# Kernel tuning notes

Hardware: AMD Instinct MI355X
Metric: run time of the kernel (lower is better)

Reference implementation:

```python
import jax, jax.numpy as jnp
import numpy as np

NEG_SLOPE = 0.2  # PyG GATv2 default negative_slope


def _gru_last(x, W_ih, W_hh, b_ih, b_hh):
    """x: [B, T, Hin] -> final GRU hidden state [B, H] (torch nn.GRU equations)."""
    gx = x @ W_ih.T + b_ih  # [B, T, 3H], input gates precomputed
    H = W_hh.shape[1]

    def step(h, g):
        gh = h @ W_hh.T + b_hh
        xr, xz, xn = jnp.split(g, 3, axis=-1)
        hr, hz, hn = jnp.split(gh, 3, axis=-1)
        r = jax.nn.sigmoid(xr + hr)
        z = jax.nn.sigmoid(xz + hz)
        n = jnp.tanh(xn + r * hn)
        return (1.0 - z) * n + z * h, None

    h0 = jnp.zeros((x.shape[0], H), x.dtype)
    hT, _ = jax.lax.scan(step, h0, jnp.swapaxes(gx, 0, 1))
    return hT


def _conv(x, w, b, stride):
    y = jax.lax.conv_general_dilated(x, w, (stride, stride), 'SAME',
                                     dimension_numbers=('NCHW', 'OIHW', 'NCHW'))
    return jax.nn.relu(y + b[None, :, None, None])


def _forward(obs, phase, obs_map, edges, edges_feature, params):
    (W_nbrs, b_nbrs, W_ih, W_hh, b_ih, b_hh, Wl, Wr, att_a, gat_bias,
     conv1_w, conv1_b, conv2_w, conv2_b, Wc, bc, Wp, bp, Wh, bh,
     Wo, bo, Wa, ba) = params
    B, N = obs.shape[0], obs.shape[1]
    BN = B * N
    heads, C = att_a.shape

    # per-node obs embedding (MLP) + GRU over seq -> last hidden
    x = jax.nn.relu(obs.reshape(BN, obs.shape[2], obs.shape[3]) @ W_nbrs + b_nbrs)
    h = _gru_last(x, W_ih, W_hh, b_ih, b_hh)  # [BN, hidden]

    # flat_edges: offset each sample's node ids by b*N, concat along edge dim
    offsets = (jnp.arange(B) * N)[:, None, None]
    ei = (edges + offsets).transpose(1, 0, 2).reshape(2, -1)  # [2, B*E]
    loops = jnp.arange(BN)  # PyG GATv2 add_self_loops=True
    src = jnp.concatenate([ei[0], loops])
    dst = jnp.concatenate([ei[1], loops])

    # GATv2Conv (heads, concat=False): gather -> leakyrelu -> edge softmax -> scatter
    xl = (h @ Wl).reshape(BN, heads, C)
    xr = (h @ Wr).reshape(BN, heads, C)
    e = jax.nn.leaky_relu(xl[src] + xr[dst], NEG_SLOPE)  # [Etot, heads, C]
    logits = jnp.einsum('ehc,hc->eh', e, att_a)          # [Etot, heads]
    m = jax.ops.segment_max(logits, dst, num_segments=BN)
    p = jnp.exp(logits - m[dst])
    s = jax.ops.segment_sum(p, dst, num_segments=BN)
    alpha = p / s[dst]                                    # [Etot, heads]
    node_out = jax.ops.segment_sum(xl[src] * alpha[..., None], dst, num_segments=BN)
    obs_gat = node_out.mean(axis=1) + gat_bias            # concat=False -> head mean

    source_idx = jnp.arange(B) * N  # ego intersection of each sample
    obs_gat = obs_gat[source_idx]   # [B, hidden]

    # CNNBase on map
    c = _conv(obs_map, conv1_w, conv1_b, 2)
    c = _conv(c, conv2_w, conv2_b, 2)
    target_emb = jax.nn.relu(c.reshape(B, -1) @ Wc + bc)

    # phase MLP, fusion MLP, dueling head
    phase_emb = jax.nn.relu(phase @ Wp + bp)
    fused = jnp.concatenate([obs_gat, target_emb, phase_emb], axis=1)
    hid = jax.nn.relu(fused @ Wh + bh)
    v = hid @ Wo + bo
    adv = hid @ Wa + ba
    out = v + (adv - adv.mean(axis=-1, keepdims=True))
    return out, alpha


def setup_inputs() -> dict:
    key = jax.random.key(0)
    B, N, T, Fo = 16, 1000, 16, 16      # batch, n_nodes, seq_len, obs_length+4
    H, heads, P, A, E = 128, 5, 8, 8, 4000
    Cm, HW = 4, 32
    ks = iter(jax.random.split(key, 40))

    def rn(shape, scale=0.05):
        return jax.random.normal(next(ks), shape, dtype=jnp.float32) * scale

    return dict(
        obs=rn((B, N, T, Fo), 1.0),
        phase=rn((B, P), 1.0),
        obs_map=rn((B, Cm, HW, HW), 1.0),
        edges=jax.random.randint(next(ks), (B, 2, E), 0, N),
        edges_feature=rn((B, E, 4), 1.0),
        W_nbrs=rn((Fo, H)), b_nbrs=jnp.zeros((H,), jnp.float32),
        W_ih=rn((3 * H, H)), W_hh=rn((3 * H, H)),
        b_ih=jnp.zeros((3 * H,), jnp.float32), b_hh=jnp.zeros((3 * H,), jnp.float32),
        Wl=rn((H, heads * H)), Wr=rn((H, heads * H)),
        att_a=rn((heads, H)), gat_bias=jnp.zeros((H,), jnp.float32),
        conv1_w=rn((32, Cm, 3, 3)), conv1_b=jnp.zeros((32,), jnp.float32),
        conv2_w=rn((64, 32, 3, 3)), conv2_b=jnp.zeros((64,), jnp.float32),
        Wc=rn((64 * (HW // 4) * (HW // 4), H)), bc=jnp.zeros((H,), jnp.float32),
        Wp=rn((P, P)), bp=jnp.zeros((P,), jnp.float32),
        Wh=rn((2 * H + P, H)), bh=jnp.zeros((H,), jnp.float32),
        Wo=rn((H, 1)), bo=jnp.zeros((1,), jnp.float32),
        Wa=rn((H, A)), ba=jnp.zeros((A,), jnp.float32),
    )


def reference(obs, phase, obs_map, edges, edges_feature,
              W_nbrs, b_nbrs, W_ih, W_hh, b_ih, b_hh,
              Wl, Wr, att_a, gat_bias,
              conv1_w, conv1_b, conv2_w, conv2_b, Wc, bc,
              Wp, bp, Wh, bh, Wo, bo, Wa, ba):
    params = (W_nbrs, b_nbrs, W_ih, W_hh, b_ih, b_hh, Wl, Wr, att_a, gat_bias,
              conv1_w, conv1_b, conv2_w, conv2_b, Wc, bc, Wp, bp, Wh, bh,
              Wo, bo, Wa, ba)
    return _forward(obs, phase, obs_map, edges, edges_feature, params)
```

## Files before the change

### kernel.cpp

```cpp
#include <hip/hip_runtime.h>
#include <hip/hip_bf16.h>
#include <math.h>

#define B_    16
#define N_    1000
#define BN_   16000
#define T_    16
#define FO    16
#define H_    128
#define G3    384
#define HEADS 5
#define HC    640
#define E_    4000
#define EG    64000
#define ETOT  80000
#define P_    8
#define A_    8
#define NEG_SLOPE 0.2f

typedef __attribute__((ext_vector_type(8))) short bf16x8;
typedef __attribute__((ext_vector_type(4))) float f32x4;

__device__ __forceinline__ float bf2f(unsigned short u){ return __uint_as_float(((unsigned)u)<<16); }
__device__ __forceinline__ unsigned short f2bf(float x){
    unsigned u = __float_as_uint(x);
    unsigned r = (u + 0x7FFFu + ((u>>16)&1u)) >> 16;
    return (unsigned short)r;
}
__device__ __forceinline__ unsigned cvtpk(float lo, float hi){
    unsigned r;
    asm volatile("v_cvt_pk_bf16_f32 %0, %1, %2" : "=v"(r) : "v"(lo), "v"(hi));
    return r;
}
__device__ __forceinline__ float rcpf(float x){ return __builtin_amdgcn_rcpf(x); }

__global__ __launch_bounds__(256) void k_prep_c1(
        const float* __restrict__ Wih, const float* __restrict__ Whh,
        const float* __restrict__ Wl, const float* __restrict__ Wr,
        const float* __restrict__ Wn, const float* __restrict__ bn,
        unsigned short* __restrict__ Wihb, unsigned short* __restrict__ Whhb,
        unsigned short* __restrict__ WTb, unsigned short* __restrict__ WnTb,
        float* __restrict__ segsum, float* __restrict__ node_out,
        float* __restrict__ tacc,
        const float* __restrict__ im, const float* __restrict__ w1,
        const float* __restrict__ b1, float* __restrict__ c1out){
    __shared__ float sW[32*4*9];
    int t = threadIdx.x;
    if(blockIdx.x < 640){
        int i = blockIdx.x*256 + t;
        if(i < G3*H_){ Wihb[i] = f2bf(Wih[i]); Whhb[i] = f2bf(Whh[i]); }
        if(i < 2*HC*H_){
            int c = i >> 7, k = i & 127;
            float v = (c < HC) ? Wl[(size_t)k*HC + c] : Wr[(size_t)k*HC + (c-HC)];
            WTb[i] = f2bf(v);
        }
        if(i < H_*32){
            int c = i >> 5, k = i & 31;
            WnTb[i] = (k < FO) ? f2bf(Wn[k*H_ + c])
                     : (k == FO ? f2bf(bn[c]) : (unsigned short)0);
        }
        if(i < BN_*HEADS) segsum[i] = 0.0f;
        if(i < B_*HC) node_out[i] = 0.0f;
        if(i < B_*H_) tacc[i] = 0.0f;
    } else {
        for(int i=t;i<32*4*9;i+=256) sW[i]=w1[i];
        __syncthreads();
        int idx = (blockIdx.x-640)*256 + t;
        int ox = idx & 15, oy = (idx>>4)&15, oc = (idx>>8)&31, b = idx>>13;
        float acc = b1[oc];
        for(int ic=0;ic<4;ic++){
            const float* ip = &im[(size_t)((b*4+ic)*32)*32];
            const float* wp = &sW[(oc*4+ic)*9];
            #pragma unroll
            for(int ky=0;ky<3;ky++){
                int iy = oy*2+ky; if(iy>=32) continue;
                #pragma unroll
                for(int kx=0;kx<3;kx++){
                    int ix = ox*2+kx; if(ix>=32) continue;
                    acc = fmaf(ip[iy*32+ix], wp[ky*3+kx], acc);
                }
            }
        }
        c1out[idx] = fmaxf(acc, 0.f);
    }
}

__global__ __launch_bounds__(512,2) void k_gruf(const float* __restrict__ obs,
        const unsigned short* __restrict__ WnTb,
        const unsigned short* __restrict__ Wihb, const float* __restrict__ bih,
        const unsigned short* __restrict__ Whhb, const float* __restrict__ bhh,
        unsigned short* __restrict__ hout,
        const float* __restrict__ c1, const float* __restrict__ w2,
        const float* __restrict__ b2, float* __restrict__ c2out){
    __shared__ unsigned short sX[2*8192];
    __shared__ unsigned short sH[2*8192];
    int t = threadIdx.x;

    if(blockIdx.x >= 250){
        int idx = (blockIdx.x-250)*512 + t;
        int ox = idx & 7, oy = (idx>>3)&7, oc = (idx>>6)&63, b = idx>>12;
        float acc = b2[oc];
        for(int ic=0;ic<32;ic++){
            const float* ip = &c1[(size_t)((b*32+ic)*16)*16];
            const float* wp = &w2[(oc*32+ic)*9];
            #pragma unroll
            for(int ky=0;ky<3;ky++){
                int iy = oy*2+ky; if(iy>=16) continue;
                #pragma unroll
                for(int kx=0;kx<3;kx++){
                    int ix = ox*2+kx; if(ix>=16) continue;
                    acc = fmaf(ip[iy*16+ix], wp[ky*3+kx], acc);
                }
            }
        }
        c2out[idx] = fmaxf(acc, 0.f);
        return;
    }

    int w = t>>6, lane = t&63, lq = lane>>4, lm = lane&15;

    bf16x8 wfi[3][4], wfh[3][4];
    #pragma unroll
    for(int i=0;i<3;i++){
        int row = (8*i + w)*16 + lm;
        #pragma unroll
        for(int kt=0;kt<4;kt++){
            wfi[i][kt] = *(const bf16x8*)&Wihb[row*H_ + kt*32 + lq*8];
            wfh[i][kt] = *(const bf16x8*)&Whhb[row*H_ + kt*32 + lq*8];
        }
    }
    bf16x8 wfn = *(const bf16x8*)&WnTb[(w*16+lm)*32 + lq*8];
    int cb = w*16 + lq*4;
    f32x4 b_r, b_z, bxn, bhn;
    { f32x4 t1=*(const f32x4*)&bih[cb],     t2=*(const f32x4*)&bhh[cb];     b_r=t1+t2; }
    { f32x4 t1=*(const f32x4*)&bih[128+cb], t2=*(const f32x4*)&bhh[128+cb]; b_z=t1+t2; }
    bxn = *(const f32x4*)&bih[256+cb];
    bhn = *(const f32x4*)&bhh[256+cb];

    int rd[4];
    #pragma unroll
    for(int kt=0;kt<4;kt++) rd[kt] = lm*128 + (((4*kt+lq)^(lm&7))<<3);
    const int wrt = lm*128 + (((2*w + (lq>>1))^(lm&7))<<3) + ((lq&1)<<2);

    int nodeBase = blockIdx.x*64;
    const float* obp0 = &obs[(size_t)(nodeBase + lm)*256 + lq*8];

    for(int i=t;i<4096;i+=512) ((unsigned*)sH)[i] = 0u;
    float ho[4][4] = {{0.f,0.f,0.f,0.f},{0.f,0.f,0.f,0.f},
                      {0.f,0.f,0.f,0.f},{0.f,0.f,0.f,0.f}};

    float4 oA[4], oB[4];
    if(lq < 2){
        #pragma unroll
        for(int g=0; g<4; g++){
            const float* q = obp0 + (size_t)g*16*256;
            oA[g] = *(const float4*)(q);    oB[g] = *(const float4*)(q+4);
        }
    }
    #pragma unroll
    for(int g=0; g<4; g++){
        bf16x8 ob = (bf16x8){0,0,0,0,0,0,0,0};
        if(lq < 2){
            union { uint4 u; bf16x8 v; } cv;
            cv.u = make_uint4(cvtpk(oA[g].x,oA[g].y), cvtpk(oA[g].z,oA[g].w),
                              cvtpk(oB[g].x,oB[g].y), cvtpk(oB[g].z,oB[g].w));
            ob = cv.v;
        } else if(lq == 2){
            ob[0] = (short)0x3F80;
        }
        f32x4 xa = (f32x4){0.f,0.f,0.f,0.f};
        xa = __builtin_amdgcn_mfma_f32_16x16x32_bf16(wfn, ob, xa, 0,0,0);
        unsigned u0 = cvtpk(fmaxf(xa[0],0.f), fmaxf(xa[1],0.f));
        unsigned u1 = cvtpk(fmaxf(xa[2],0.f), fmaxf(xa[3],0.f));
        *(uint2*)&sX[g*2048 + wrt] = make_uint2(u0,u1);
    }
    __syncthreads();

    int p = 0;
    #pragma unroll 1
    for(int s=0; s<T_; s++){
        if(s < T_-1 && lq < 2){
            #pragma unroll
            for(int g=0; g<4; g++){
                const float* q = obp0 + (size_t)g*16*256 + (s+1)*16;
                oA[g] = *(const float4*)(q);    oB[g] = *(const float4*)(q+4);
            }
        }
        #pragma unroll
        for(int g=0; g<4; g++){
            int base = p*8192 + g*2048;
            bf16x8 xb[4], hb[4];
            #pragma unroll
            for(int kt=0;kt<4;kt++){
                xb[kt] = *(const bf16x8*)&sX[base + rd[kt]];
                hb[kt] = *(const bf16x8*)&sH[base + rd[kt]];
            }
            f32x4 ar = b_r, az = b_z, axi = bxn, ahh = bhn;
            #pragma unroll
            for(int kt=0;kt<4;kt++){
                ar  = __builtin_amdgcn_mfma_f32_16x16x32_bf16(wfi[0][kt], xb[kt], ar, 0,0,0);
                az  = __builtin_amdgcn_mfma_f32_16x16x32_bf16(wfi[1][kt], xb[kt], az, 0,0,0);
                axi = __builtin_amdgcn_mfma_f32_16x16x32_bf16(wfi[2][kt], xb[kt], axi, 0,0,0);
                ar  = __builtin_amdgcn_mfma_f32_16x16x32_bf16(wfh[0][kt], hb[kt], ar, 0,0,0);
                az  = __builtin_amdgcn_mfma_f32_16x16x32_bf16(wfh[1][kt], hb[kt], az, 0,0,0);
                ahh = __builtin_amdgcn_mfma_f32_16x16x32_bf16(wfh[2][kt], hb[kt], ahh, 0,0,0);
            }
            #pragma unroll
            for(int v=0;v<4;v++){
                float er = __expf(-ar[v]);
                float r  = rcpf(1.f + er);
                float ez = __expf(-az[v]);
                float z  = rcpf(1.f + ez);
                float xn = fmaf(r, ahh[v], axi[v]);
                float en = __expf(-2.f*xn);
                float nn = fmaf(2.f, rcpf(1.f + en), -1.f);
                ho[g][v] = nn + z*(ho[g][v] - nn);
            }
            unsigned u0 = cvtpk(ho[g][0], ho[g][1]);
            unsigned u1 = cvtpk(ho[g][2], ho[g][3]);
            *(uint2*)&sH[(p^1)*8192 + g*2048 + wrt] = make_uint2(u0,u1);
        }
        if(s < T_-1){
            #pragma unroll
            for(int g=0; g<4; g++){
                bf16x8 ob = (bf16x8){0,0,0,0,0,0,0,0};
                if(lq < 2){
                    union { uint4 u; bf16x8 v; } cv;
                    cv.u = make_uint4(cvtpk(oA[g].x,oA[g].y), cvtpk(oA[g].z,oA[g].w),
                                      cvtpk(oB[g].x,oB[g].y), cvtpk(oB[g].z,oB[g].w));
                    ob = cv.v;
                } else if(lq == 2){
                    ob[0] = (short)0x3F80;
                }
                f32x4 xa = (f32x4){0.f,0.f,0.f,0.f};
                xa = __builtin_amdgcn_mfma_f32_16x16x32_bf16(wfn, ob, xa, 0,0,0);
                unsigned u0 = cvtpk(fmaxf(xa[0],0.f), fmaxf(xa[1],0.f));
                unsigned u1 = cvtpk(fmaxf(xa[2],0.f), fmaxf(xa[3],0.f));
                *(uint2*)&sX[(p^1)*8192 + g*2048 + wrt] = make_uint2(u0,u1);
            }
        }
        __syncthreads();
        p ^= 1;
    }
    #pragma unroll
    for(int g=0; g<4; g++){
        unsigned u0 = cvtpk(ho[g][0], ho[g][1]);
        unsigned u1 = cvtpk(ho[g][2], ho[g][3]);
        *(uint2*)&hout[(size_t)(nodeBase + g*16 + lm)*H_ + cb] = make_uint2(u0,u1);
    }
}

__global__ __launch_bounds__(256) void k_xlxr(const unsigned short* __restrict__ hb16,
        const unsigned short* __restrict__ WTb,
        unsigned short* __restrict__ xl, unsigned short* __restrict__ xr){
    int t = threadIdx.x;
    int w = t>>6, lane = t&63, lq = lane>>4, lm = lane&15;
    int nb = blockIdx.x / 5, cgrp = blockIdx.x % 5;
    int nblk = nb*128;
    int ct0 = cgrp*16 + w*4;
    bf16x8 wf[4][4];
    #pragma unroll
    for(int i=0;i<4;i++){
        int row = (ct0+i)*16 + lm;
        #pragma unroll
        for(int kt=0;kt<4;kt++)
            wf[i][kt] = *(const bf16x8*)&WTb[(size_t)row*H_ + kt*32 + lq*8];
    }
    for(int g=0; g<8; g++){
        int node = nblk + g*16 + lm;
        bf16x8 hb[4];
        #pragma unroll
        for(int kt=0;kt<4;kt++)
            hb[kt] = *(const bf16x8*)&hb16[(size_t)node*H_ + kt*32 + lq*8];
        f32x4 acc[4];
        #pragma unroll
        for(int i=0;i<4;i++) acc[i] = (f32x4){0.f,0.f,0.f,0.f};
        #pragma unroll
        for(int kt=0;kt<4;kt++){
            #pragma unroll
            for(int i=0;i<4;i++)
                acc[i] = __builtin_amdgcn_mfma_f32_16x16x32_bf16(wf[i][kt], hb[kt], acc[i], 0,0,0);
        }
        #pragma unroll
        for(int i=0;i<4;i++){
            int col = (ct0+i)*16 + lq*4;
            ushort4 o;
            o.x=f2bf(acc[i][0]); o.y=f2bf(acc[i][1]); o.z=f2bf(acc[i][2]); o.w=f2bf(acc[i][3]);
            if(col < HC) *(ushort4*)&xl[(size_t)node*HC + col] = o;
            else         *(ushort4*)&xr[(size_t)node*HC + (col-HC)] = o;
        }
    }
}

__device__ __forceinline__ void edge_sd(int e, const int* __restrict__ edges, int* src, int* dst){
    if(e < EG){
        int b = e / E_, j = e - b*E_;
        *src = edges[(b*2+0)*E_ + j] + b*N_;
        *dst = edges[(b*2+1)*E_ + j] + b*N_;
    } else { *src = *dst = e - EG; }
}

__global__ __launch_bounds__(256) void k_logits_tb(const unsigned short* __restrict__ xl,
        const unsigned short* __restrict__ xr, const int* __restrict__ edges,
        const float* __restrict__ atta, float* __restrict__ pbuf,
        float* __restrict__ segsum,
        const float* __restrict__ c2, const float* __restrict__ Wc,
        float* __restrict__ tacc){
    __shared__ float sC[128];
    int t = threadIdx.x;
    if(blockIdx.x < 5000){
        int lb = (blockIdx.x & 7)*625 + (blockIdx.x >> 3);
        int lane = t & 63, w = t >> 6;
        float am[8], a4[8];
        #pragma unroll
        for(int j=0;j<8;j++) am[j] = atta[lane*8+j];
        #pragma unroll
        for(int j=0;j<8;j++) a4[j] = (lane<16) ? atta[512+lane*8+j] : 0.f;

        int e0 = lb*16 + w*4;
        int srcs[4], dsts[4];
        #pragma unroll
        for(int i=0;i<4;i++) edge_sd(e0+i, edges, &srcs[i], &dsts[i]);
        #pragma unroll
        for(int i=0;i<4;i++){
            const unsigned short* xls = &xl[(size_t)srcs[i]*HC];
            const unsigned short* xrd = &xr[(size_t)dsts[i]*HC];
            uint4 ul = *(const uint4*)&xls[lane*8];
            uint4 ur = *(const uint4*)&xrd[lane*8];
            uint4 tl = make_uint4(0,0,0,0), tr = make_uint4(0,0,0,0);
            if(lane < 16){
                tl = *(const uint4*)&xls[512+lane*8];
                tr = *(const uint4*)&xrd[512+lane*8];
            }
            float pm = 0.f, p4 = 0.f;
            {
                unsigned pl[4] = {ul.x,ul.y,ul.z,ul.w};
                unsigned pr[4] = {ur.x,ur.y,ur.z,ur.w};
                #pragma unroll
                for(int q=0;q<4;q++){
                    float s0 = bf2f((unsigned short)(pl[q]&0xFFFFu)) + bf2f((unsigned short)(pr[q]&0xFFFFu));
                    float s1 = bf2f((unsigned short)(pl[q]>>16))     + bf2f((unsigned short)(pr[q]>>16));
                    s0 = s0 > 0.f ? s0 : NEG_SLOPE*s0;
                    s1 = s1 > 0.f ? s1 : NEG_SLOPE*s1;
                    pm = fmaf(s0, am[2*q],   pm);
                    pm = fmaf(s1, am[2*q+1], pm);
                }
            }
            {
                unsigned ql[4] = {tl.x,tl.y,tl.z,tl.w};
                unsigned qr[4] = {tr.x,tr.y,tr.z,tr.w};
                #pragma unroll
                for(int q=0;q<4;q++){
                    float s0 = bf2f((unsigned short)(ql[q]&0xFFFFu)) + bf2f((unsigned short)(qr[q]&0xFFFFu));
                    float s1 = bf2f((unsigned short)(ql[q]>>16))     + bf2f((unsigned short)(qr[q]>>16));
                    s0 = s0 > 0.f ? s0 : NEG_SLOPE*s0;
                    s1 = s1 > 0.f ? s1 : NEG_SLOPE*s1;
                    p4 = fmaf(s0, a4[2*q],   p4);
                    p4 = fmaf(s1, a4[2*q+1], p4);
                }
            }
            #pragma unroll
            for(int off=1; off<16; off<<=1){
                pm += __shfl_xor(pm, off);
                p4 += __shfl_xor(p4, off);
            }
            if((lane & 15) == 0){
                int hh = lane >> 4;
                float p = __expf(pm);
                pbuf[(size_t)(e0+i)*HEADS + hh] = p;
                atomicAdd(&segsum[dsts[i]*HEADS + hh], p);
            }
            if(lane == 8){
                float p = __expf(p4);
                pbuf[(size_t)(e0+i)*HEADS + 4] = p;
                atomicAdd(&segsum[dsts[i]*HEADS + 4], p);
            }
        }
    } else {
        int bb = blockIdx.x - 5000;
        int b = bb >> 5, ks = bb & 31;
        int k0 = ks*128;
        if(t < 128) sC[t] = c2[(size_t)b*4096 + k0 + t];
        __syncthreads();
        int j = t & 127, sub = t >> 7;
        const float* wp = &Wc[(size_t)(k0 + sub*64)*H_ + j];
        const float* cp = &sC[sub*64];
        float a0=0.f, a1=0.f, a2=0.f, a3=0.f;
        #pragma unroll
        for(int kk=0; kk<64; kk+=4){
            a0 = fmaf(cp[kk+0], wp[(size_t)(kk+0)*H_], a0);
            a1 = fmaf(cp[kk+1], wp[(size_t)(kk+1)*H_], a1);
            a2 = fmaf(cp[kk+2], wp[(size_t)(kk+2)*H_], a2);
            a3 = fmaf(cp[kk+3], wp[(size_t)(kk+3)*H_], a3);
        }
        atomicAdd(&tacc[b*H_+j], (a0+a1)+(a2+a3));
    }
}

__global__ void k_alpha(const float* __restrict__ pbuf, const float* __restrict__ segsum,
                        const int* __restrict__ edges, const unsigned short* __restrict__ xl,
                        float* __restrict__ out_alpha, float* __restrict__ node_out){
    int idx = blockIdx.x*256 + threadIdx.x;
    int lane = threadIdx.x & 63;
    bool valid = idx < ETOT*HEADS;
    int e = 0, hh = 0, src = 0, dst = 0;
    float a = 0.f;
    bool ego = false;
    if(valid){
        e = idx / HEADS; hh = idx - e*HEADS;
        edge_sd(e, edges, &src, &dst);
        a = pbuf[idx] / segsum[dst*HEADS + hh];
        out_alpha[idx] = a;
        ego = (dst % N_) == 0;
    }
    unsigned long long m = __ballot(ego);
    while(m){
        int l = __ffsll((unsigned long long)m) - 1;
        m &= (m - 1);
        float aa = __shfl(a, l);
        int ss = __shfl(src, l), dd = __shfl(dst, l), hq = __shfl(hh, l);
        int b = dd / N_;
        unsigned u = *(const unsigned*)&xl[(size_t)ss*HC + hq*H_ + lane*2];
        float* no = &node_out[b*HC + hq*H_ + lane*2];
        atomicAdd(no,     aa * bf2f((unsigned short)(u & 0xFFFFu)));
        atomicAdd(no + 1, aa * bf2f((unsigned short)(u >> 16)));
    }
}

__global__ __launch_bounds__(256) void k_head(const float* __restrict__ node_out,
        const float* __restrict__ gat_bias, const float* __restrict__ tacc,
        const float* __restrict__ bc, const float* __restrict__ phase,
        const float* __restrict__ Wp, const float* __restrict__ bp,
        const float* __restrict__ Wh, const float* __restrict__ bh,
        const float* __restrict__ Wo, const float* __restrict__ bo,
        const float* __restrict__ Wa, const float* __restrict__ ba,
        float* __restrict__ out){
    __shared__ float sF[268];
    __shared__ float sHid[128];
    int t = threadIdx.x;
    int b = blockIdx.x;
    if(t < 128){
        float s=0.f;
        #pragma unroll
        for(int hh=0;hh<HEADS;hh++) s += node_out[b*HC + hh*H_ + t];
        sF[t] = s*(1.0f/HEADS) + gat_bias[t];
    } else {
        int c = t - 128;
        sF[128+c] = fmaxf(tacc[b*H_ + c] + bc[c], 0.f);
    }
    if(t < P_){
        float s=bp[t];
        #pragma unroll
        for(int q=0;q<P_;q++) s = fmaf(phase[b*P_+q], Wp[q*P_+t], s);
        sF[256+t] = fmaxf(s, 0.f);
    }
    __syncthreads();
    if(t < 128){
        float s=bh[t];
        for(int k=0;k<2*H_+P_;k++) s = fmaf(sF[k], Wh[k*H_+t], s);
        sHid[t]=fmaxf(s,0.f);
    }
    __syncthreads();
    if(t < A_){
        float v=bo[0], ad=ba[t];
        for(int k=0;k<H_;k++){ float hv=sHid[k]; v = fmaf(hv,Wo[k],v); ad = fmaf(hv,Wa[k*A_+t],ad); }
        float m = ad;
        m += __shfl_xor(m,1); m += __shfl_xor(m,2); m += __shfl_xor(m,4);
        m *= 0.125f;
        out[b*A_+t] = v + ad - m;
    }
}

extern "C" void kernel_launch(void* const* d_in, const int* in_sizes, int n_in,
                              void* d_out, int out_size, void* d_ws, size_t ws_size,
                              hipStream_t stream) {
    (void)in_sizes; (void)n_in; (void)out_size; (void)ws_size;
    const float* obs      = (const float*)d_in[0];
    const float* phase    = (const float*)d_in[1];
    const float* obs_map  = (const float*)d_in[2];
    const int*   edges    = (const int*)  d_in[3];
    const float* W_nbrs   = (const float*)d_in[5];
    const float* b_nbrs   = (const float*)d_in[6];
    const float* W_ih     = (const float*)d_in[7];
    const float* W_hh     = (const float*)d_in[8];
    const float* b_ih     = (const float*)d_in[9];
    const float* b_hh     = (const float*)d_in[10];
    const float* Wl       = (const float*)d_in[11];
    const float* Wr       = (const float*)d_in[12];
    const float* att_a    = (const float*)d_in[13];
    const float* gat_bias = (const float*)d_in[14];
    const float* conv1_w  = (const float*)d_in[15];
    const float* conv1_b  = (const float*)d_in[16];
    const float* conv2_w  = (const float*)d_in[17];
    const float* conv2_b  = (const float*)d_in[18];
    const float* Wc       = (const float*)d_in[19];
    const float* bc       = (const float*)d_in[20];
    const float* Wp       = (const float*)d_in[21];
    const float* bp       = (const float*)d_in[22];
    const float* Wh       = (const float*)d_in[23];
    const float* bh       = (const float*)d_in[24];
    const float* Wo       = (const float*)d_in[25];
    const float* bo       = (const float*)d_in[26];
    const float* Wa       = (const float*)d_in[27];
    const float* ba       = (const float*)d_in[28];

    float* out = (float*)d_out;
    float* w   = (float*)d_ws;

    size_t off = 0;
    unsigned short* hbuf = (unsigned short*)(w + off); off += (size_t)BN_*H_/2;
    unsigned short* xl   = (unsigned short*)(w + off); off += (size_t)BN_*HC/2;
    unsigned short* xr   = (unsigned short*)(w + off); off += (size_t)BN_*HC/2;
    float* pbuf   = w + off; off += (size_t)ETOT*HEADS;
    float* segsum = w + off; off += (size_t)BN_*HEADS;
    float* nodeo  = w + off; off += (size_t)B_*HC;
    float* c1     = w + off; off += (size_t)16*32*16*16;
    float* c2     = w + off; off += (size_t)16*64*8*8;
    float* tacc   = w + off; off += (size_t)B_*H_;
    unsigned short* Wihb = (unsigned short*)(w + off); off += (size_t)H_*G3/2;
    unsigned short* Whhb = (unsigned short*)(w + off); off += (size_t)H_*G3/2;
    unsigned short* WTb  = (unsigned short*)(w + off); off += (size_t)2*HC*H_/2;
    unsigned short* WnTb = (unsigned short*)(w + off); off += (size_t)H_*32/2;

    k_prep_c1<<<640 + 512, 256, 0, stream>>>(W_ih, W_hh, Wl, Wr, W_nbrs, b_nbrs,
                                             Wihb, Whhb, WTb, WnTb,
                                             segsum, nodeo, tacc,
                                             obs_map, conv1_w, conv1_b, c1);

    k_gruf<<<250 + 128, 512, 0, stream>>>(obs, WnTb, Wihb, b_ih, Whhb, b_hh, hbuf,
                                          c1, conv2_w, conv2_b, c2);

    k_xlxr<<<625, 256, 0, stream>>>(hbuf, WTb, xl, xr);

    k_logits_tb<<<5000 + 512, 256, 0, stream>>>(xl, xr, edges, att_a, pbuf, segsum,
                                                c2, Wc, tacc);

    k_alpha<<<(ETOT*HEADS+255)/256, 256, 0, stream>>>(pbuf, segsum, edges, xl, out+128, nodeo);

    k_head<<<B_, 256, 0, stream>>>(nodeo, gat_bias, tacc, bc, phase,
                                   Wp, bp, Wh, bh, Wo, bo, Wa, ba, out);
}
```

Before: 177.9 us.

## Fuse xl/xr projection into GRU kernel epilogue and split conv2 out

```diff
diff --git a/kernel.cpp b/kernel.cpp
--- a/kernel.cpp
+++ b/kernel.cpp
@@ -89,34 +89,11 @@
         const unsigned short* __restrict__ WnTb,
         const unsigned short* __restrict__ Wihb, const float* __restrict__ bih,
         const unsigned short* __restrict__ Whhb, const float* __restrict__ bhh,
-        unsigned short* __restrict__ hout,
-        const float* __restrict__ c1, const float* __restrict__ w2,
-        const float* __restrict__ b2, float* __restrict__ c2out){
+        const unsigned short* __restrict__ WTb,
+        unsigned short* __restrict__ xl, unsigned short* __restrict__ xr){
     __shared__ unsigned short sX[2*8192];
     __shared__ unsigned short sH[2*8192];
     int t = threadIdx.x;
-
-    if(blockIdx.x >= 250){
-        int idx = (blockIdx.x-250)*512 + t;
-        int ox = idx & 7, oy = (idx>>3)&7, oc = (idx>>6)&63, b = idx>>12;
-        float acc = b2[oc];
-        for(int ic=0;ic<32;ic++){
-            const float* ip = &c1[(size_t)((b*32+ic)*16)*16];
-            const float* wp = &w2[(oc*32+ic)*9];
-            #pragma unroll
-            for(int ky=0;ky<3;ky++){
-                int iy = oy*2+ky; if(iy>=16) continue;
-                #pragma unroll
-                for(int kx=0;kx<3;kx++){
-                    int ix = ox*2+kx; if(ix>=16) continue;
-                    acc = fmaf(ip[iy*16+ix], wp[ky*3+kx], acc);
-                }
-            }
-        }
-        c2out[idx] = fmaxf(acc, 0.f);
-        return;
-    }
-
     int w = t>>6, lane = t&63, lq = lane>>4, lm = lane&15;
 
     bf16x8 wfi[3][4], wfh[3][4];
@@ -242,54 +219,58 @@
         __syncthreads();
         p ^= 1;
     }
+
+    bf16x8 hba[4][4];
     #pragma unroll
-    for(int g=0; g<4; g++){
-        unsigned u0 = cvtpk(ho[g][0], ho[g][1]);
-        unsigned u1 = cvtpk(ho[g][2], ho[g][3]);
-        *(uint2*)&hout[(size_t)(nodeBase + g*16 + lm)*H_ + cb] = make_uint2(u0,u1);
-    }
-}
-
-__global__ __launch_bounds__(256) void k_xlxr(const unsigned short* __restrict__ hb16,
-        const unsigned short* __restrict__ WTb,
-        unsigned short* __restrict__ xl, unsigned short* __restrict__ xr){
-    int t = threadIdx.x;
-    int w = t>>6, lane = t&63, lq = lane>>4, lm = lane&15;
-    int nb = blockIdx.x / 5, cgrp = blockIdx.x % 5;
-    int nblk = nb*128;
-    int ct0 = cgrp*16 + w*4;
-    bf16x8 wf[4][4];
-    #pragma unroll
-    for(int i=0;i<4;i++){
-        int row = (ct0+i)*16 + lm;
+    for(int g=0;g<4;g++){
         #pragma unroll
         for(int kt=0;kt<4;kt++)
-            wf[i][kt] = *(const bf16x8*)&WTb[(size_t)row*H_ + kt*32 + lq*8];
-    }
-    for(int g=0; g<8; g++){
-        int node = nblk + g*16 + lm;
-        bf16x8 hb[4];
+            hba[g][kt] = *(const bf16x8*)&sH[p*8192 + g*2048 + rd[kt]];
+    }
+    #pragma unroll 1
+    for(int tt=0; tt<10; tt++){
+        int tile = w + tt*8;
+        int row = tile*16 + lm;
+        bf16x8 wf[4];
         #pragma unroll
         for(int kt=0;kt<4;kt++)
-            hb[kt] = *(const bf16x8*)&hb16[(size_t)node*H_ + kt*32 + lq*8];
-        f32x4 acc[4];
-        #pragma unroll
-        for(int i=0;i<4;i++) acc[i] = (f32x4){0.f,0.f,0.f,0.f};
-        #pragma unroll
-        for(int kt=0;kt<4;kt++){
-            #pragma unroll
-            for(int i=0;i<4;i++)
-                acc[i] = __builtin_amdgcn_mfma_f32_16x16x32_bf16(wf[i][kt], hb[kt], acc[i], 0,0,0);
-        }
-        #pragma unroll
-        for(int i=0;i<4;i++){
-            int col = (ct0+i)*16 + lq*4;
+            wf[kt] = *(const bf16x8*)&WTb[(size_t)row*H_ + kt*32 + lq*8];
+        #pragma unroll
+        for(int g=0;g<4;g++){
+            f32x4 acc = (f32x4){0.f,0.f,0.f,0.f};
+            #pragma unroll
+            for(int kt=0;kt<4;kt++)
+                acc = __builtin_amdgcn_mfma_f32_16x16x32_bf16(wf[kt], hba[g][kt], acc, 0,0,0);
+            int node = nodeBase + g*16 + lm;
+            int col = tile*16 + lq*4;
             ushort4 o;
-            o.x=f2bf(acc[i][0]); o.y=f2bf(acc[i][1]); o.z=f2bf(acc[i][2]); o.w=f2bf(acc[i][3]);
+            o.x=f2bf(acc[0]); o.y=f2bf(acc[1]); o.z=f2bf(acc[2]); o.w=f2bf(acc[3]);
             if(col < HC) *(ushort4*)&xl[(size_t)node*HC + col] = o;
             else         *(ushort4*)&xr[(size_t)node*HC + (col-HC)] = o;
         }
     }
+}
+
+__global__ __launch_bounds__(256) void k_conv2(const float* __restrict__ c1,
+        const float* __restrict__ w, const float* __restrict__ bias, float* __restrict__ outp){
+    int idx = blockIdx.x*256 + threadIdx.x;
+    if(idx >= 16*64*8*8) return;
+    int ox = idx & 7, oy = (idx>>3)&7, oc = (idx>>6)&63, b = idx>>12;
+    float acc = bias[oc];
+    for(int ic=0;ic<32;ic++){
+        const float* ip = &c1[(size_t)((b*32+ic)*16)*16];
+        const float* wp = &w[(oc*32+ic)*9];
+        #pragma unroll
+        for(int ky=0;ky<3;ky++){
+            int iy = oy*2+ky; if(iy>=16) continue;
+            #pragma unroll
+            for(int kx=0;kx<3;kx++){
+                int ix = ox*2+kx; if(ix>=16) continue;
+                acc = fmaf(ip[iy*16+ix], wp[ky*3+kx], acc);
+            }
+        }
+    }
+    outp[idx] = fmaxf(acc, 0.f);
 }
 
 __device__ __forceinline__ void edge_sd(int e, const int* __restrict__ edges, int* src, int* dst){
@@ -508,7 +489,6 @@
     float* w   = (float*)d_ws;
 
     size_t off = 0;
-    unsigned short* hbuf = (unsigned short*)(w + off); off += (size_t)BN_*H_/2;
     unsigned short* xl   = (unsigned short*)(w + off); off += (size_t)BN_*HC/2;
     unsigned short* xr   = (unsigned short*)(w + off); off += (size_t)BN_*HC/2;
     float* pbuf   = w + off; off += (size_t)ETOT*HEADS;
@@ -527,10 +507,9 @@
                                              segsum, nodeo, tacc,
                                              obs_map, conv1_w, conv1_b, c1);
 
-    k_gruf<<<250 + 128, 512, 0, stream>>>(obs, WnTb, Wihb, b_ih, Whhb, b_hh, hbuf,
-                                          c1, conv2_w, conv2_b, c2);
-
-    k_xlxr<<<625, 256, 0, stream>>>(hbuf, WTb, xl, xr);
+    k_gruf<<<250, 512, 0, stream>>>(obs, WnTb, Wihb, b_ih, Whhb, b_hh, WTb, xl, xr);
+
+    k_conv2<<<(16*64*8*8)/256, 256, 0, stream>>>(c1, conv2_w, conv2_b, c2);
 
     k_logits_tb<<<5000 + 512, 256, 0, stream>>>(xl, xr, edges, att_a, pbuf, segsum,
                                                 c2, Wc, tacc);
```

New measurement: 166.7 us. -6.3%, faster.
